# Kernel tuning notes

Measured on AMD Instinct MI355X. Metric: run time of the kernel, lower is better.

Reference implementation:

```python
import jax, jax.numpy as jnp
import numpy as np

B, N, D = 2, 2048, 768
HEADS, DIM_HEAD = 12, 64
INNER = HEADS * DIM_HEAD  # 768
OUT_DIM = 768


def setup_inputs() -> dict:
    key = jax.random.key(0)
    k1, k2, k3, k4, k5 = jax.random.split(key, 5)
    s_in = 1.0 / np.sqrt(D)
    s_inner = 1.0 / np.sqrt(INNER)
    return {
        "x": jax.random.normal(k1, (B, N, D), dtype=jnp.float32),
        "w_qkv": jax.random.normal(k2, (D, 3 * INNER), dtype=jnp.float32) * s_in,
        "b_qkv": jax.random.normal(k3, (3 * INNER,), dtype=jnp.float32) * 0.01,
        "w_out": jax.random.normal(k4, (INNER, OUT_DIM), dtype=jnp.float32) * s_inner,
        "b_out": jax.random.normal(k5, (OUT_DIM,), dtype=jnp.float32) * 0.01,
    }


def reference(x, w_qkv, b_qkv, w_out, b_out):
    b, n, _ = x.shape
    scale = DIM_HEAD ** -0.5
    qkv = x @ w_qkv + b_qkv                      # [b, n, 3*inner]
    q, k, v = jnp.split(qkv, 3, axis=-1)
    # 'b n (h d) -> b h n d'
    reshape = lambda t: t.reshape(b, n, HEADS, DIM_HEAD).transpose(0, 2, 1, 3)
    q, k, v = reshape(q), reshape(k), reshape(v)
    dots = jnp.einsum("bhnd,bhmd->bhnm", q, k) * scale
    attn = jax.nn.softmax(dots, axis=-1)
    out = jnp.einsum("bhnm,bhmd->bhnd", attn, v)  # [b, h, n, d]
    out = out.transpose(0, 2, 1, 3).reshape(b, n, INNER)
    return out @ w_out + b_out
```

## Files before the change

kernel.cpp:

```cpp
#include <hip/hip_runtime.h>
#include <hip/hip_bf16.h>
#include <stdint.h>


typedef __attribute__((ext_vector_type(8))) short bf16x8;
typedef __attribute__((ext_vector_type(4))) float f32x4;
typedef __attribute__((address_space(3))) unsigned int lds_uint;
typedef __attribute__((address_space(1))) const unsigned int g_uint;

__device__ __forceinline__ short f2bf(float f) {
    union { float f; uint32_t u; } x; x.f = f;
    uint32_t r = (x.u + 0x7fffu + ((x.u >> 16) & 1u)) >> 16;
    return (short)r;
}
__device__ __forceinline__ float exp2fast(float x) {
#if __has_builtin(__builtin_amdgcn_exp2f)
    return __builtin_amdgcn_exp2f(x);
#else
    return __expf(x * 0.6931471805599453f);
#endif
}
__device__ __forceinline__ void gl_lds16(const void* g, void* l) {
    __builtin_amdgcn_global_load_lds((g_uint*)g, (lds_uint*)l, 16, 0, 0);
}
#define WAITCNT_VM(N) asm volatile("s_waitcnt vmcnt(" #N ")" ::: "memory")
#define BARRIER_FENCED() do { __builtin_amdgcn_s_barrier(); \
                              asm volatile("" ::: "memory"); } while (0)

__device__ __forceinline__ void tr_tile(const float* __restrict__ W,
                                        short* __restrict__ Wt, int K, int N,
                                        int n0, int k0, int t, short* S) {
    {
        int kl = t >> 2, ng = t & 3;
        const float* src = W + (size_t)(k0 + kl) * N + n0 + ng * 16;
        #pragma unroll
        for (int j = 0; j < 16; j += 4) {
            float4 f = *(const float4*)(src + j);
            S[(ng*16 + j + 0) * 65 + kl] = f2bf(f.x);
            S[(ng*16 + j + 1) * 65 + kl] = f2bf(f.y);
            S[(ng*16 + j + 2) * 65 + kl] = f2bf(f.z);
            S[(ng*16 + j + 3) * 65 + kl] = f2bf(f.w);
        }
    }
    __syncthreads();
    {
        int nl = t >> 2, kg = t & 3;
        short* dst = Wt + (size_t)(n0 + nl) * K + k0 + kg * 16;
        #pragma unroll
        for (int j = 0; j < 16; j += 4) {
            short4 s4;
            s4.x = S[nl*65 + kg*16 + j + 0];
            s4.y = S[nl*65 + kg*16 + j + 1];
            s4.z = S[nl*65 + kg*16 + j + 2];
            s4.w = S[nl*65 + kg*16 + j + 3];
            *(short4*)(dst + j) = s4;
        }
    }
}

__global__ __launch_bounds__(256)
void prep_k(const float* __restrict__ x, short* __restrict__ Xb,
            const float* __restrict__ Wq, short* __restrict__ Wqt,
            const float* __restrict__ Wo, short* __restrict__ Wot)
{
    __shared__ short S[64 * 65];
    const int t = threadIdx.x;
    if (blockIdx.x < 1536) {
        int i = (blockIdx.x * 256 + t) * 8;
        float4 f0 = *(const float4*)(x + i);
        float4 f1 = *(const float4*)(x + i + 4);
        short s[8];
        s[0]=f2bf(f0.x); s[1]=f2bf(f0.y); s[2]=f2bf(f0.z); s[3]=f2bf(f0.w);
        s[4]=f2bf(f1.x); s[5]=f2bf(f1.y); s[6]=f2bf(f1.z); s[7]=f2bf(f1.w);
        *(uint4*)(Xb + i) = *(uint4*)s;
        return;
    }
    if (blockIdx.x < 1968) {
        const int b2 = blockIdx.x - 1536;
        tr_tile(Wq, Wqt, 768, 2304, (b2 % 36) * 64, (b2 / 36) * 64, t, S);
    } else {
        const int b3 = blockIdx.x - 1968;
        tr_tile(Wo, Wot, 768, 768, (b3 % 12) * 64, (b3 / 12) * 64, t, S);
    }
}

__global__ __launch_bounds__(256)
void tr_w(const float* __restrict__ W, short* __restrict__ Wt, int K, int N) {
    __shared__ short S[64 * 65];
    tr_tile(W, Wt, K, N, blockIdx.x * 64, blockIdx.y * 64, threadIdx.x, S);
}

__global__ __launch_bounds__(256)
void gemm_qkv(const short* __restrict__ A, const short* __restrict__ Bt,
              const float* __restrict__ bias,
              short* __restrict__ Qb, short* __restrict__ Kb, short* __restrict__ Vt)
{
    __shared__ short As[3][128 * 32];
    __shared__ short Bs[3][96 * 32];
    const int tid = threadIdx.x, lane = tid & 63, w = tid >> 6;
    const int wm = w >> 1, wn = w & 1, quad = lane >> 4, lcol = lane & 15;

    const int id = blockIdx.x;
    const int xcd = id & 7, j = id >> 3;
    const int bm = (xcd * 4 + (j / 24)) * 128;
    const int bn = (j % 24) * 96;

    f32x4 acc[4][3];
    #pragma unroll
    for (int i = 0; i < 4; i++)
        #pragma unroll
        for (int jj = 0; jj < 3; jj++) acc[i][jj] = (f32x4){0.f, 0.f, 0.f, 0.f};

    const int ar0 = tid >> 2,         ac0 = (tid & 3) * 8;
    const int ar1 = (tid + 256) >> 2;
    const int c2  = 256 + tid;
    const int br1 = c2 >> 2,          bc1 = (c2 & 3) * 8;

    const short* pA0 = A  + (size_t)(bm + ar0) * 768 + ac0;
    const short* pA1 = A  + (size_t)(bm + ar1) * 768 + ac0;
    const short* pB0 = Bt + (size_t)(bn + ar0) * 768 + ac0;
    const short* pB1 = Bt + (size_t)(bn + br1) * 768 + bc1;

    #pragma unroll
    for (int t0 = 0; t0 < 2; t0++) {
        const int kt = t0 * 32;
        gl_lds16(pA0 + kt, As[t0] + tid * 8);
        gl_lds16(pA1 + kt, As[t0] + (tid + 256) * 8);
        gl_lds16(pB0 + kt, Bs[t0] + tid * 8);
        if (tid < 128)
            gl_lds16(pB1 + kt, Bs[t0] + c2 * 8);
    }
    if (w < 2) { WAITCNT_VM(4); } else { WAITCNT_VM(3); }
    BARRIER_FENCED();

    #pragma unroll
    for (int it = 0; it < 24; it++) {
        const int p = it % 3;
        if (it < 22) {
            const int pb = (it + 2) % 3, kt = (it + 2) * 32;
            gl_lds16(pA0 + kt, As[pb] + tid * 8);
            gl_lds16(pA1 + kt, As[pb] + (tid + 256) * 8);
            gl_lds16(pB0 + kt, Bs[pb] + tid * 8);
            if (tid < 128)
                gl_lds16(pB1 + kt, Bs[pb] + c2 * 8);
        }
        bf16x8 a[4], b[3];
        #pragma unroll
        for (int tm = 0; tm < 4; tm++)
            a[tm] = *(const bf16x8*)(As[p] + (wm*64 + tm*16 + lcol) * 32 + quad * 8);
        #pragma unroll
        for (int tn = 0; tn < 3; tn++)
            b[tn] = *(const bf16x8*)(Bs[p] + (wn*48 + tn*16 + lcol) * 32 + quad * 8);
        #pragma unroll
        for (int tm = 0; tm < 4; tm++)
            #pragma unroll
            for (int tn = 0; tn < 3; tn++)
                acc[tm][tn] = __builtin_amdgcn_mfma_f32_16x16x32_bf16(a[tm], b[tn], acc[tm][tn], 0, 0, 0);
        if (it < 23) {
            if (it < 22) {
                if (w < 2) { WAITCNT_VM(4); } else { WAITCNT_VM(3); }
            } else {
                WAITCNT_VM(0);
            }
            BARRIER_FENCED();
        }
    }

    const float SCLQ = 0.18033688011112042f;
    #pragma unroll
    for (int tm = 0; tm < 4; tm++) {
        #pragma unroll
        for (int tn = 0; tn < 3; tn++) {
            int col = bn + wn*48 + tn*16 + lcol;
            float bv = bias[col];
            int which = (col >= 1536) ? 2 : (col >= 768 ? 1 : 0);
            int cc = col - which * 768;
            int h = cc >> 6, d = cc & 63;
            int rowbase = bm + wm*64 + tm*16 + quad*4;
            int bb = rowbase >> 11, n0 = rowbase & 2047;
            int bh = bb * 12 + h;
            if (which == 2) {
                short4 s4;
                s4.x = f2bf(acc[tm][tn][0] + bv);
                s4.y = f2bf(acc[tm][tn][1] + bv);
                s4.z = f2bf(acc[tm][tn][2] + bv);
                s4.w = f2bf(acc[tm][tn][3] + bv);
                *(short4*)(Vt + (((size_t)bh*32 + (n0 >> 6))*64 + d)*64 + (n0 & 63)) = s4;
            } else {
                #pragma unroll
                for (int reg = 0; reg < 4; reg++) {
                    float v = acc[tm][tn][reg] + bv;
                    if (which == 0) v *= SCLQ;
                    short* dst = (which == 0) ? Qb : Kb;
                    dst[((size_t)bh*2048 + n0 + reg)*64 + d] = f2bf(v);
                }
            }
        }
    }
}

#define ATTN_STEP(P, PB, DO_PRE, WMODE) do {                                   \
    if (DO_PRE) {                                                              \
        gl_lds16(pK0, Ks[PB] + c0 * 8);                                        \
        gl_lds16(pV0, Vs[PB] + c0 * 8);                                        \
        gl_lds16(pK1, Ks[PB] + c1 * 8);                                        \
        gl_lds16(pV1, Vs[PB] + c1 * 8);                                        \
        pK0 += 4096; pV0 += 4096; pK1 += 4096; pV1 += 4096;                    \
    }                                                                          \
    f32x4 st[4];                                                               \
    _Pragma("unroll")                                                          \
    for (int kvs = 0; kvs < 4; kvs++) st[kvs] = (f32x4){0.f, 0.f, 0.f, 0.f};   \
    _Pragma("unroll")                                                          \
    for (int ks = 0; ks < 2; ks++) {                                           \
        _Pragma("unroll")                                                      \
        for (int kvs = 0; kvs < 4; kvs++) {                                    \
            bf16x8 kf = *(const bf16x8*)(Ks[P] + (kvs*16 + lcol) * 64 +        \
                                         (((ks*4 + quad) ^ ksw) << 3));        \
            st[kvs] = __builtin_amdgcn_mfma_f32_16x16x32_bf16(kf, qf[ks],      \
                                                              st[kvs], 0, 0, 0); \
        }                                                                      \
    }                                                                          \
    uint32_t X[4], Y[4];                                                       \
    _Pragma("unroll")                                                          \
    for (int kvs = 0; kvs < 4; kvs++) {                                        \
        float p0 = exp2fast(st[kvs][0]), p1 = exp2fast(st[kvs][1]);            \
        float p2 = exp2fast(st[kvs][2]), p3 = exp2fast(st[kvs][3]);            \
        lp += (p0 + p1) + (p2 + p3);                                           \
        asm("v_cvt_pk_bf16_f32 %0, %1, %2" : "=v"(X[kvs]) : "v"(p0), "v"(p1)); \
        asm("v_cvt_pk_bf16_f32 %0, %1, %2" : "=v"(Y[kvs]) : "v"(p2), "v"(p3)); \
    }                                                                          \
    bf16x8 pa[2];                                                              \
    _Pragma("unroll")                                                          \
    for (int ks = 0; ks < 2; ks++) {                                           \
        uint32_t a0 = X[2*ks], a1 = X[2*ks + 1];                               \
        uint32_t b0 = Y[2*ks], b1 = Y[2*ks + 1];                               \
        asm("v_permlane16_swap_b32 %0, %1" : "+v"(a0), "+v"(a1));              \
        asm("v_permlane16_swap_b32 %0, %1" : "+v"(b0), "+v"(b1));              \
        union { uint32_t u[4]; bf16x8 v; } pk_;                                \
        pk_.u[0] = a0; pk_.u[1] = b0; pk_.u[2] = a1; pk_.u[3] = b1;            \
        pa[ks] = pk_.v;                                                        \
    }                                                                          \
    _Pragma("unroll")                                                          \
    for (int ks = 0; ks < 2; ks++) {                                           \
        _Pragma("unroll")                                                      \
        for (int tn = 0; tn < 4; tn++) {                                       \
            int row = tn * 16 + lcol;                                          \
            bf16x8 bv = *(const bf16x8*)(Vs[P] + row * 64 +                    \
                                         (((ks*4 + bq) ^ (row & 7)) << 3));    \
            o[tn] = __builtin_amdgcn_mfma_f32_16x16x32_bf16(pa[ks], bv,        \
                                                            o[tn], 0, 0, 0);   \
        }                                                                      \
    }                                                                          \
    if (WMODE == 0) { WAITCNT_VM(4); BARRIER_FENCED(); }                       \
    else if (WMODE == 1) { WAITCNT_VM(0); BARRIER_FENCED(); }                  \
} while (0)

__global__ __launch_bounds__(256)
void attn_k(const short* __restrict__ Q, const short* __restrict__ K,
            const short* __restrict__ Vt, short* __restrict__ Ab)
{
    __shared__ __align__(16) short Ks[3][4096];
    __shared__ __align__(16) short Vs[3][4096];

    const int tid = threadIdx.x, lane = tid & 63, w = tid >> 6;
    const int quad = lane >> 4, lcol = lane & 15;
    const int bid = blockIdx.x;
    const int bh = bid % 24, qt = bid / 24;
    const int b = bh / 12, h = bh - b * 12;

    const short* Kg = K  + (size_t)bh * 131072;
    const short* Vg = Vt + (size_t)bh * 131072;

    bf16x8 qf[2];
    {
        const short* Qg = Q + ((size_t)bh * 2048 + (size_t)qt * 64) * 64;
        #pragma unroll
        for (int ks = 0; ks < 2; ks++)
            qf[ks] = *(const bf16x8*)(Qg + (w*16 + lcol) * 64 + ks*32 + quad*8);
    }

    const int c0 = tid, c1 = tid + 256;
    const int r0 = c0 >> 3, s0 = r0 * 64 + (((c0 & 7) ^ (r0 & 7)) << 3);
    const int r1 = c1 >> 3, s1 = r1 * 64 + (((c1 & 7) ^ (r1 & 7)) << 3);

    #pragma unroll
    for (int t0 = 0; t0 < 2; t0++) {
        gl_lds16(Kg + t0 * 4096 + s0, Ks[t0] + c0 * 8);
        gl_lds16(Vg + t0 * 4096 + s0, Vs[t0] + c0 * 8);
        gl_lds16(Kg + t0 * 4096 + s1, Ks[t0] + c1 * 8);
        gl_lds16(Vg + t0 * 4096 + s1, Vs[t0] + c1 * 8);
    }
    WAITCNT_VM(4);
    BARRIER_FENCED();

    const short* pK0 = Kg + 2 * 4096 + s0;
    const short* pV0 = Vg + 2 * 4096 + s0;
    const short* pK1 = Kg + 2 * 4096 + s1;
    const short* pV1 = Vg + 2 * 4096 + s1;

    f32x4 o[4];
    #pragma unroll
    for (int tn = 0; tn < 4; tn++) o[tn] = (f32x4){0.f, 0.f, 0.f, 0.f};
    float lp = 0.f;

    const int ksw = lcol & 7;
    const int bq  = ((quad & 1) << 1) | (quad >> 1);

    for (int g = 0; g < 10; g++) {
        ATTN_STEP(0, 2, true, 0);
        ATTN_STEP(1, 0, true, 0);
        ATTN_STEP(2, 1, true, 0);
    }
    ATTN_STEP(0, 0, false, 1);
    ATTN_STEP(1, 0, false, 2);

    lp += __shfl_xor(lp, 16, 64);
    lp += __shfl_xor(lp, 32, 64);
    float rl[4];
    #pragma unroll
    for (int r = 0; r < 4; r++)
        rl[r] = 1.0f / __shfl(lp, quad * 4 + r, 64);

    #pragma unroll
    for (int tn = 0; tn < 4; tn++) {
        #pragma unroll
        for (int r = 0; r < 4; r++) {
            int q = qt * 64 + w * 16 + quad * 4 + r;
            int d = h * 64 + tn * 16 + lcol;
            Ab[((size_t)(b * 2048 + q)) * 768 + d] = f2bf(o[tn][r] * rl[r]);
        }
    }
}

__global__ __launch_bounds__(256)
void gemm_out(const short* __restrict__ A, const short* __restrict__ Bt,
              const float* __restrict__ bias, float* __restrict__ Of)
{
    __shared__ short As[5][64 * 32];
    __shared__ short Bs[5][96 * 32];
    const int tid = threadIdx.x, lane = tid & 63, w = tid >> 6;
    const int wm = w >> 1, wn = w & 1, quad = lane >> 4, lcol = lane & 15;

    const int id = blockIdx.x;
    const int xcd = id & 7, j = id >> 3;
    const int bm = (xcd * 8 + (j >> 3)) * 64;
    const int bn = (j & 7) * 96;

    f32x4 acc[2][3];
    #pragma unroll
    for (int i = 0; i < 2; i++)
        #pragma unroll
        for (int jj = 0; jj < 3; jj++) acc[i][jj] = (f32x4){0.f, 0.f, 0.f, 0.f};

    const int ar0 = tid >> 2, ac0 = (tid & 3) * 8;
    const int c2  = 256 + tid;
    const int br1 = c2 >> 2,  bc1 = (c2 & 3) * 8;

    const short* pA0 = A  + (size_t)(bm + ar0) * 768 + ac0;
    const short* pB0 = Bt + (size_t)(bn + ar0) * 768 + ac0;
    const short* pB1 = Bt + (size_t)(bn + br1) * 768 + bc1;

    #pragma unroll
    for (int t0 = 0; t0 < 3; t0++) {
        const int kt = t0 * 32;
        gl_lds16(pA0 + kt, As[t0] + tid * 8);
        gl_lds16(pB0 + kt, Bs[t0] + tid * 8);
        if (tid < 128)
            gl_lds16(pB1 + kt, Bs[t0] + c2 * 8);
    }
    if (w < 2) { WAITCNT_VM(3); } else { WAITCNT_VM(2); }
    BARRIER_FENCED();

    #pragma unroll
    for (int it = 0; it < 24; it++) {
        const int p = it % 5;
        if (it < 21) {
            const int pb = (it + 3) % 5, kt = (it + 3) * 32;
            gl_lds16(pA0 + kt, As[pb] + tid * 8);
            gl_lds16(pB0 + kt, Bs[pb] + tid * 8);
            if (tid < 128)
                gl_lds16(pB1 + kt, Bs[pb] + c2 * 8);
        }
        bf16x8 a[2], b[3];
        #pragma unroll
        for (int tm = 0; tm < 2; tm++)
            a[tm] = *(const bf16x8*)(As[p] + (wm*32 + tm*16 + lcol) * 32 + quad * 8);
        #pragma unroll
        for (int tn = 0; tn < 3; tn++)
            b[tn] = *(const bf16x8*)(Bs[p] + (wn*48 + tn*16 + lcol) * 32 + quad * 8);
        #pragma unroll
        for (int tm = 0; tm < 2; tm++)
            #pragma unroll
            for (int tn = 0; tn < 3; tn++)
                acc[tm][tn] = __builtin_amdgcn_mfma_f32_16x16x32_bf16(a[tm], b[tn], acc[tm][tn], 0, 0, 0);
        if ((it & 1) && it <= 21) {
            if (it < 21) {
                if (w < 2) { WAITCNT_VM(3); } else { WAITCNT_VM(2); }
            } else {
                WAITCNT_VM(0);
            }
            BARRIER_FENCED();
        }
    }
    #pragma unroll
    for (int tm = 0; tm < 2; tm++) {
        #pragma unroll
        for (int tn = 0; tn < 3; tn++) {
            int col = bn + wn*48 + tn*16 + lcol;
            float bv = bias[col];
            #pragma unroll
            for (int reg = 0; reg < 4; reg++) {
                int row = bm + wm*32 + tm*16 + quad*4 + reg;
                Of[(size_t)row * 768 + col] = acc[tm][tn][reg] + bv;
            }
        }
    }
}

extern "C" void kernel_launch(void* const* d_in, const int* in_sizes, int n_in,
                              void* d_out, int out_size, void* d_ws, size_t ws_size,
                              hipStream_t stream)
{
    (void)in_sizes; (void)n_in; (void)out_size;
    const float* x     = (const float*)d_in[0];
    const float* w_qkv = (const float*)d_in[1];
    const float* b_qkv = (const float*)d_in[2];
    const float* w_out = (const float*)d_in[3];
    const float* b_out = (const float*)d_in[4];
    float* out = (float*)d_out;

    const size_t XSZ = (size_t)4096 * 768;
    const size_t WQ  = (size_t)2304 * 768;
    const size_t WO  = (size_t)768 * 768;
    const size_t HSZ = (size_t)24 * 2048 * 64;
    short* Xb  = (short*)d_ws;
    short* Wqt = Xb + XSZ;
    short* Qb  = Wqt + WQ;
    short* Kb  = Qb + HSZ;
    short* Vt  = Kb + HSZ;
    short* Ab  = Xb;

    const bool sepWot = ws_size >= (XSZ + WQ + 3*HSZ + WO) * sizeof(short);
    short* Wot = sepWot ? (Vt + HSZ) : Wqt;

    if (sepWot) {
        prep_k<<<2112, 256, 0, stream>>>(x, Xb, w_qkv, Wqt, w_out, Wot);
        gemm_qkv<<<768, 256, 0, stream>>>(Xb, Wqt, b_qkv, Qb, Kb, Vt);
    } else {
        prep_k<<<1968, 256, 0, stream>>>(x, Xb, w_qkv, Wqt, w_out, Wot);
        gemm_qkv<<<768, 256, 0, stream>>>(Xb, Wqt, b_qkv, Qb, Kb, Vt);
        tr_w<<<dim3(12, 12), 256, 0, stream>>>(w_out, Wot, 768, 768);
    }
    attn_k<<<768, 256, 0, stream>>>(Qb, Kb, Vt, Ab);
    gemm_out<<<512, 256, 0, stream>>>(Ab, Wot, b_out, out);
}
```

Before: 152.1 us.

## Fuse x fp32-to-bf16 conversion into QKV GEMM A-tile loads

Removes the separate pass in prep_k that converted x to bf16 and wrote it to workspace. The QKV GEMM now loads fp32 x through registers, converts it in-kernel, and stores it into the LDS A buffers, while B still uses direct global-to-LDS loads. The pipeline's wait logic moves from vmcnt counting to lgkmcnt waits. This saves a full write and re-read of X, but each of the 24 N-tile blocks now re-reads fp32 x at twice the bytes and repeats the conversion, and register-staged loads may hide latency less well.

```diff
diff --git a/kernel.cpp b/kernel.cpp
--- a/kernel.cpp
+++ b/kernel.cpp
@@ -24,6 +24,7 @@
     __builtin_amdgcn_global_load_lds((g_uint*)g, (lds_uint*)l, 16, 0, 0);
 }
 #define WAITCNT_VM(N) asm volatile("s_waitcnt vmcnt(" #N ")" ::: "memory")
+#define WAITCNT_LGKM0() asm volatile("s_waitcnt lgkmcnt(0)" ::: "memory")
 #define BARRIER_FENCED() do { __builtin_amdgcn_s_barrier(); \
                               asm volatile("" ::: "memory"); } while (0)
 
@@ -59,27 +60,16 @@
 }
 
 __global__ __launch_bounds__(256)
-void prep_k(const float* __restrict__ x, short* __restrict__ Xb,
-            const float* __restrict__ Wq, short* __restrict__ Wqt,
+void prep_k(const float* __restrict__ Wq, short* __restrict__ Wqt,
             const float* __restrict__ Wo, short* __restrict__ Wot)
 {
     __shared__ short S[64 * 65];
     const int t = threadIdx.x;
-    if (blockIdx.x < 1536) {
-        int i = (blockIdx.x * 256 + t) * 8;
-        float4 f0 = *(const float4*)(x + i);
-        float4 f1 = *(const float4*)(x + i + 4);
-        short s[8];
-        s[0]=f2bf(f0.x); s[1]=f2bf(f0.y); s[2]=f2bf(f0.z); s[3]=f2bf(f0.w);
-        s[4]=f2bf(f1.x); s[5]=f2bf(f1.y); s[6]=f2bf(f1.z); s[7]=f2bf(f1.w);
-        *(uint4*)(Xb + i) = *(uint4*)s;
-        return;
-    }
-    if (blockIdx.x < 1968) {
-        const int b2 = blockIdx.x - 1536;
+    if (blockIdx.x < 432) {
+        const int b2 = blockIdx.x;
         tr_tile(Wq, Wqt, 768, 2304, (b2 % 36) * 64, (b2 / 36) * 64, t, S);
     } else {
-        const int b3 = blockIdx.x - 1968;
+        const int b3 = blockIdx.x - 432;
         tr_tile(Wo, Wot, 768, 768, (b3 % 12) * 64, (b3 / 12) * 64, t, S);
     }
 }
@@ -90,8 +80,19 @@
     tr_tile(W, Wt, K, N, blockIdx.x * 64, blockIdx.y * 64, threadIdx.x, S);
 }
 
+#define QKV_WRITE_A(BUF, F00, F01, F10, F11) do {                              \
+    short s0[8];                                                               \
+    s0[0]=f2bf(F00.x); s0[1]=f2bf(F00.y); s0[2]=f2bf(F00.z); s0[3]=f2bf(F00.w);\
+    s0[4]=f2bf(F01.x); s0[5]=f2bf(F01.y); s0[6]=f2bf(F01.z); s0[7]=f2bf(F01.w);\
+    *(uint4*)(As[BUF] + tid * 8) = *(uint4*)s0;                                \
+    short s1[8];                                                               \
+    s1[0]=f2bf(F10.x); s1[1]=f2bf(F10.y); s1[2]=f2bf(F10.z); s1[3]=f2bf(F10.w);\
+    s1[4]=f2bf(F11.x); s1[5]=f2bf(F11.y); s1[6]=f2bf(F11.z); s1[7]=f2bf(F11.w);\
+    *(uint4*)(As[BUF] + (tid + 256) * 8) = *(uint4*)s1;                        \
+} while (0)
+
 __global__ __launch_bounds__(256)
-void gemm_qkv(const short* __restrict__ A, const short* __restrict__ Bt,
+void gemm_qkv(const float* __restrict__ X, const short* __restrict__ Bt,
               const float* __restrict__ bias,
               short* __restrict__ Qb, short* __restrict__ Kb, short* __restrict__ Vt)
 {
@@ -116,33 +117,34 @@
     const int c2  = 256 + tid;
     const int br1 = c2 >> 2,          bc1 = (c2 & 3) * 8;
 
-    const short* pA0 = A  + (size_t)(bm + ar0) * 768 + ac0;
-    const short* pA1 = A  + (size_t)(bm + ar1) * 768 + ac0;
+    const float* pX0 = X  + (size_t)(bm + ar0) * 768 + ac0;
+    const float* pX1 = X  + (size_t)(bm + ar1) * 768 + ac0;
     const short* pB0 = Bt + (size_t)(bn + ar0) * 768 + ac0;
     const short* pB1 = Bt + (size_t)(bn + br1) * 768 + bc1;
 
-    #pragma unroll
-    for (int t0 = 0; t0 < 2; t0++) {
-        const int kt = t0 * 32;
-        gl_lds16(pA0 + kt, As[t0] + tid * 8);
-        gl_lds16(pA1 + kt, As[t0] + (tid + 256) * 8);
-        gl_lds16(pB0 + kt, Bs[t0] + tid * 8);
-        if (tid < 128)
-            gl_lds16(pB1 + kt, Bs[t0] + c2 * 8);
-    }
-    if (w < 2) { WAITCNT_VM(4); } else { WAITCNT_VM(3); }
+    float4 a00 = *(const float4*)(pX0 + 0),  a01 = *(const float4*)(pX0 + 4);
+    float4 a10 = *(const float4*)(pX1 + 0),  a11 = *(const float4*)(pX1 + 4);
+    gl_lds16(pB0 + 0, Bs[0] + tid * 8);
+    if (tid < 128) gl_lds16(pB1 + 0, Bs[0] + c2 * 8);
+    float4 b00 = *(const float4*)(pX0 + 32), b01 = *(const float4*)(pX0 + 36);
+    float4 b10 = *(const float4*)(pX1 + 32), b11 = *(const float4*)(pX1 + 36);
+    gl_lds16(pB0 + 32, Bs[1] + tid * 8);
+    if (tid < 128) gl_lds16(pB1 + 32, Bs[1] + c2 * 8);
+    QKV_WRITE_A(0, a00, a01, a10, a11);
+    QKV_WRITE_A(1, b00, b01, b10, b11);
+    WAITCNT_LGKM0();
     BARRIER_FENCED();
 
     #pragma unroll
     for (int it = 0; it < 24; it++) {
         const int p = it % 3;
+        float4 c00, c01, c10, c11;
         if (it < 22) {
-            const int pb = (it + 2) % 3, kt = (it + 2) * 32;
-            gl_lds16(pA0 + kt, As[pb] + tid * 8);
-            gl_lds16(pA1 + kt, As[pb] + (tid + 256) * 8);
-            gl_lds16(pB0 + kt, Bs[pb] + tid * 8);
-            if (tid < 128)
-                gl_lds16(pB1 + kt, Bs[pb] + c2 * 8);
+            const int kt = (it + 2) * 32;
+            c00 = *(const float4*)(pX0 + kt); c01 = *(const float4*)(pX0 + kt + 4);
+            c10 = *(const float4*)(pX1 + kt); c11 = *(const float4*)(pX1 + kt + 4);
+            gl_lds16(pB0 + kt, Bs[(it + 2) % 3] + tid * 8);
+            if (tid < 128) gl_lds16(pB1 + kt, Bs[(it + 2) % 3] + c2 * 8);
         }
         bf16x8 a[4], b[3];
         #pragma unroll
@@ -156,12 +158,11 @@
             #pragma unroll
             for (int tn = 0; tn < 3; tn++)
                 acc[tm][tn] = __builtin_amdgcn_mfma_f32_16x16x32_bf16(a[tm], b[tn], acc[tm][tn], 0, 0, 0);
+        if (it < 22)
+            QKV_WRITE_A((it + 2) % 3, c00, c01, c10, c11);
         if (it < 23) {
-            if (it < 22) {
-                if (w < 2) { WAITCNT_VM(4); } else { WAITCNT_VM(3); }
-            } else {
-                WAITCNT_VM(0);
-            }
+            WAITCNT_LGKM0();
+            if (it == 22) WAITCNT_VM(0);
             BARRIER_FENCED();
         }
     }
@@ -429,26 +430,25 @@
     const float* b_out = (const float*)d_in[4];
     float* out = (float*)d_out;
 
-    const size_t XSZ = (size_t)4096 * 768;
+    const size_t ABZ = (size_t)4096 * 768;
     const size_t WQ  = (size_t)2304 * 768;
     const size_t WO  = (size_t)768 * 768;
     const size_t HSZ = (size_t)24 * 2048 * 64;
-    short* Xb  = (short*)d_ws;
-    short* Wqt = Xb + XSZ;
+    short* Ab  = (short*)d_ws;
+    short* Wqt = Ab + ABZ;
     short* Qb  = Wqt + WQ;
     short* Kb  = Qb + HSZ;
     short* Vt  = Kb + HSZ;
-    short* Ab  = Xb;
-
-    const bool sepWot = ws_size >= (XSZ + WQ + 3*HSZ + WO) * sizeof(short);
+
+    const bool sepWot = ws_size >= (ABZ + WQ + 3*HSZ + WO) * sizeof(short);
     short* Wot = sepWot ? (Vt + HSZ) : Wqt;
 
     if (sepWot) {
-        prep_k<<<2112, 256, 0, stream>>>(x, Xb, w_qkv, Wqt, w_out, Wot);
-        gemm_qkv<<<768, 256, 0, stream>>>(Xb, Wqt, b_qkv, Qb, Kb, Vt);
+        prep_k<<<576, 256, 0, stream>>>(w_qkv, Wqt, w_out, Wot);
+        gemm_qkv<<<768, 256, 0, stream>>>(x, Wqt, b_qkv, Qb, Kb, Vt);
     } else {
-        prep_k<<<1968, 256, 0, stream>>>(x, Xb, w_qkv, Wqt, w_out, Wot);
-        gemm_qkv<<<768, 256, 0, stream>>>(Xb, Wqt, b_qkv, Qb, Kb, Vt);
+        prep_k<<<432, 256, 0, stream>>>(w_qkv, Wqt, w_out, Wot);
+        gemm_qkv<<<768, 256, 0, stream>>>(x, Wqt, b_qkv, Qb, Kb, Vt);
         tr_w<<<dim3(12, 12), 256, 0, stream>>>(w_out, Wot, 768, 768);
     }
     attn_k<<<768, 256, 0, stream>>>(Qb, Kb, Vt, Ab);
```

New measurement: 156.2 us. +2.7%, slower.
